# Optimization experiments

Hardware: AMD Instinct MI355X
Metric: run time of the kernel (lower is better)

## Reference

```python
import jax, jax.numpy as jnp
import numpy as np

N_EMBD = 768
N_HEAD = 12


def setup_inputs() -> dict:
    key = jax.random.key(0)
    ks = jax.random.split(key, 5)
    B, T, C = 2, 4096, N_EMBD
    s = 1.0 / np.sqrt(C)
    x = jax.random.normal(ks[0], (B, T, C), dtype=jnp.float32)
    w_attn = jax.random.normal(ks[1], (C, 3 * C), dtype=jnp.float32) * s
    b_attn = jnp.zeros((3 * C,), dtype=jnp.float32)
    w_proj = jax.random.normal(ks[2], (C, C), dtype=jnp.float32) * s
    b_proj = jnp.zeros((C,), dtype=jnp.float32)
    return {"x": x, "w_attn": w_attn, "b_attn": b_attn,
            "w_proj": w_proj, "b_proj": b_proj}


def reference(x, w_attn, b_attn, w_proj, b_proj):
    B, T, C = x.shape
    H = N_HEAD
    D = C // H  # head dim
    qkv = x @ w_attn + b_attn  # [B,T,3C]
    q, k, v = jnp.split(qkv, 3, axis=-1)
    # [B,H,T,D]
    q = q.reshape(B, T, H, D).transpose(0, 2, 1, 3)
    k = k.reshape(B, T, H, D).transpose(0, 2, 1, 3)
    v = v.reshape(B, T, H, D).transpose(0, 2, 1, 3)
    scale = 1.0 / jnp.sqrt(jnp.asarray(D, dtype=x.dtype))
    att = jnp.einsum('bhqd,bhkd->bhqk', q, k) * scale  # [B,H,T,T]
    causal = jnp.tril(jnp.ones((T, T), dtype=bool))
    att = jnp.where(causal[None, None], att, -jnp.inf)
    att = jax.nn.softmax(att, axis=-1)
    y = jnp.einsum('bhqk,bhkd->bhqd', att, v)  # [B,H,T,D]
    y = y.transpose(0, 2, 1, 3).reshape(B, T, C)
    return y @ w_proj + b_proj
```

## Files before the change

kernel.cpp:

```cpp
#include <hip/hip_runtime.h>

#define TSEQ 4096
#define CEMB 768
#define NHEAD 12

using bf16x8 = __attribute__((ext_vector_type(8))) short;
using f32x4  = __attribute__((ext_vector_type(4))) float;

#if __has_builtin(__builtin_amdgcn_exp2f)
#define EXP2(x) __builtin_amdgcn_exp2f(x)
#else
#define EXP2(x) exp2f(x)
#endif

__device__ __forceinline__ unsigned int f2bf(float f) {
    unsigned int u = __float_as_uint(f);
    return (u + 0x7fffu + ((u >> 16) & 1u)) >> 16;
}
__device__ __forceinline__ unsigned int f2bf_fast(float f) {
    return (__float_as_uint(f) + 0x8000u) >> 16;
}
__device__ __forceinline__ unsigned int cvt_pk_bf16(float lo, float hi) {
    unsigned int r;
    asm("v_cvt_pk_bf16_f32 %0, %1, %2" : "=v"(r) : "v"(lo), "v"(hi));
    return r;
}
__device__ __forceinline__ void pswap(unsigned int& d, unsigned int& s) {
    asm("v_permlane32_swap_b32 %0, %1" : "+v"(d), "+v"(s));
    asm("v_permlane16_swap_b32 %0, %1" : "+v"(d), "+v"(s));
}
__device__ __forceinline__ void async_cp16(void* lds, const void* g) {
    __builtin_amdgcn_global_load_lds(
        (const __attribute__((address_space(1))) void*)g,
        (__attribute__((address_space(3))) void*)lds, 16, 0, 0);
}

__global__ __launch_bounds__(256) void cvt_bf16(
    const float* __restrict__ X, unsigned short* __restrict__ Xb, int n8)
{
    int i = blockIdx.x * 256 + threadIdx.x;
    if (i >= n8) return;
    float4 a = *reinterpret_cast<const float4*>(&X[(size_t)i * 8]);
    float4 b = *reinterpret_cast<const float4*>(&X[(size_t)i * 8 + 4]);
    uint4 o;
    o.x = f2bf(a.x) | (f2bf(a.y) << 16);
    o.y = f2bf(a.z) | (f2bf(a.w) << 16);
    o.z = f2bf(b.x) | (f2bf(b.y) << 16);
    o.w = f2bf(b.z) | (f2bf(b.w) << 16);
    *reinterpret_cast<uint4*>(&Xb[(size_t)i * 8]) = o;
}

__global__ __launch_bounds__(256) void wtrans(
    const float* __restrict__ W, unsigned short* __restrict__ WT, int K, int N)
{
    __shared__ unsigned short tile[64][72];
    const int k0 = blockIdx.y * 64, n0 = blockIdx.x * 64;
    const int tid = threadIdx.x;
#pragma unroll
    for (int it = 0; it < 4; ++it) {
        int f = tid + it * 256;
        int r = f >> 4, c4 = f & 15;
        float4 v = *reinterpret_cast<const float4*>(&W[(size_t)(k0 + r) * N + n0 + c4 * 4]);
        tile[r][c4 * 4 + 0] = (unsigned short)f2bf(v.x);
        tile[r][c4 * 4 + 1] = (unsigned short)f2bf(v.y);
        tile[r][c4 * 4 + 2] = (unsigned short)f2bf(v.z);
        tile[r][c4 * 4 + 3] = (unsigned short)f2bf(v.w);
    }
    __syncthreads();
#pragma unroll
    for (int it = 0; it < 2; ++it) {
        int f = tid + it * 256;
        int rn = f >> 3, c8 = f & 7;
        unsigned short tmp[8];
#pragma unroll
        for (int j = 0; j < 8; ++j) tmp[j] = tile[c8 * 8 + j][rn];
        *reinterpret_cast<uint4*>(&WT[(size_t)(n0 + rn) * K + k0 + c8 * 8]) =
            *reinterpret_cast<uint4*>(tmp);
    }
}

template<int BF16OUT, int QSCALE, int VTRANS>
__global__ __launch_bounds__(256) void gemm_mfma(
    const unsigned short* __restrict__ A,
    const unsigned short* __restrict__ BT,
    const float* __restrict__ bias,
    void* __restrict__ Cv,
    unsigned short* __restrict__ VtG,
    int M, int N, int K)
{
    __shared__ __align__(16) unsigned short As[128 * 64];
    __shared__ __align__(16) unsigned short Bs[128 * 64];

    const int nwg = gridDim.x * gridDim.y;
    const int id = blockIdx.y * gridDim.x + blockIdx.x;
    const int qx = nwg >> 3;
    const int swz = (id & 7) * qx + (id >> 3);
    const int nb = N >> 7;
    const int m0 = (swz / nb) * 128, n0 = (swz % nb) * 128;

    const int tid = threadIdx.x;
    const int w = tid >> 6, lane = tid & 63;
    const int wr = w >> 1, wc = w & 1;
    const int lq = lane & 15, g = lane >> 4;
    const int wrOff = wr * 64, wcOff = wc * 64;

    f32x4 acc[4][4];
#pragma unroll
    for (int i = 0; i < 4; ++i)
#pragma unroll
        for (int j = 0; j < 4; ++j) acc[i][j] = (f32x4){0.f, 0.f, 0.f, 0.f};

    for (int k0 = 0; k0 < K; k0 += 64) {
#pragma unroll
        for (int it = 0; it < 4; ++it) {
            const int dbase = it * 256 + w * 64;
            const int d = dbase + lane;
            const int r = d >> 3;
            const int s = (d & 7) ^ (r & 7);
            async_cp16((char*)As + dbase * 16, A + (size_t)(m0 + r) * K + k0 + s * 8);
            async_cp16((char*)Bs + dbase * 16, BT + (size_t)(n0 + r) * K + k0 + s * 8);
        }
        __syncthreads();

#pragma unroll
        for (int kk = 0; kk < 2; ++kk) {
            bf16x8 af[4], bfr[4];
#pragma unroll
            for (int i = 0; i < 4; ++i) {
                const int ra = wrOff + i * 16 + lq;
                af[i] = *reinterpret_cast<const bf16x8*>(
                    (char*)As + ra * 128 + (((kk * 4 + g) ^ (ra & 7)) << 4));
                const int rb = wcOff + i * 16 + lq;
                bfr[i] = *reinterpret_cast<const bf16x8*>(
                    (char*)Bs + rb * 128 + (((kk * 4 + g) ^ (rb & 7)) << 4));
            }
#pragma unroll
            for (int i = 0; i < 4; ++i)
#pragma unroll
                for (int j = 0; j < 4; ++j)
                    acc[i][j] = __builtin_amdgcn_mfma_f32_16x16x32_bf16(
                        af[i], bfr[j], acc[i][j], 0, 0, 0);
        }
        __syncthreads();
    }

#pragma unroll
    for (int i = 0; i < 4; ++i)
#pragma unroll
        for (int j = 0; j < 4; ++j) {
            const int col = n0 + wcOff + j * 16 + lq;
            const float bv = bias[col];
            const float scl = (QSCALE && col < CEMB) ? 0.18033688011112042f : 1.0f;
            const int row0 = m0 + wrOff + i * 16 + g * 4;
            float v0 = (acc[i][j][0] + bv) * scl;
            float v1 = (acc[i][j][1] + bv) * scl;
            float v2 = (acc[i][j][2] + bv) * scl;
            float v3 = (acc[i][j][3] + bv) * scl;
            if (VTRANS && col >= 2 * CEMB) {
                const int hh = (col - 2 * CEMB) >> 6;
                const int dd = col & 63;
                uint2 pk;
                pk.x = f2bf(v0) | (f2bf(v1) << 16);
                pk.y = f2bf(v2) | (f2bf(v3) << 16);
                *reinterpret_cast<uint2*>(
                    &VtG[((size_t)(row0 >> 12) * NHEAD + hh) * 64 * TSEQ +
                         (size_t)dd * TSEQ + (row0 & 4095)]) = pk;
            } else if (BF16OUT) {
                unsigned short* Cb = (unsigned short*)Cv;
                Cb[(size_t)(row0 + 0) * N + col] = (unsigned short)f2bf(v0);
                Cb[(size_t)(row0 + 1) * N + col] = (unsigned short)f2bf(v1);
                Cb[(size_t)(row0 + 2) * N + col] = (unsigned short)f2bf(v2);
                Cb[(size_t)(row0 + 3) * N + col] = (unsigned short)f2bf(v3);
            } else {
                float* Cf = (float*)Cv;
                Cf[(size_t)(row0 + 0) * N + col] = v0;
                Cf[(size_t)(row0 + 1) * N + col] = v1;
                Cf[(size_t)(row0 + 2) * N + col] = v2;
                Cf[(size_t)(row0 + 3) * N + col] = v3;
            }
        }
}


#define QK_DUAL(SA, SB)                                                               \
{                                                                                     \
    const int xr = lq & 7;                                                            \
    _Pragma("unroll")                                                                 \
    for (int c = 0; c < 4; ++c) {                                                     \
        const int krow = 16 * c + lq;                                                 \
        bf16x8 kf0 = *reinterpret_cast<const bf16x8*>(Kb + krow * 128 + ((g ^ xr) << 4));       \
        bf16x8 kf1 = *reinterpret_cast<const bf16x8*>(Kb + krow * 128 + (((4 + g) ^ xr) << 4)); \
        f32x4 a = (f32x4){0.f, 0.f, 0.f, 0.f};                                        \
        a = __builtin_amdgcn_mfma_f32_16x16x32_bf16(kf0, qfA[0], a, 0, 0, 0);         \
        a = __builtin_amdgcn_mfma_f32_16x16x32_bf16(kf1, qfA[1], a, 0, 0, 0);         \
        SA[c] = a;                                                                    \
        f32x4 bb = (f32x4){0.f, 0.f, 0.f, 0.f};                                       \
        bb = __builtin_amdgcn_mfma_f32_16x16x32_bf16(kf0, qfB[0], bb, 0, 0, 0);       \
        bb = __builtin_amdgcn_mfma_f32_16x16x32_bf16(kf1, qfB[1], bb, 0, 0, 0);       \
        SB[c] = bb;                                                                   \
    }                                                                                 \
}

#define QK_ONE(SB, QF)                                                                \
{                                                                                     \
    const int xr = lq & 7;                                                            \
    _Pragma("unroll")                                                                 \
    for (int c = 0; c < 4; ++c) {                                                     \
        const int krow = 16 * c + lq;                                                 \
        bf16x8 kf0 = *reinterpret_cast<const bf16x8*>(Kb + krow * 128 + ((g ^ xr) << 4));       \
        bf16x8 kf1 = *reinterpret_cast<const bf16x8*>(Kb + krow * 128 + (((4 + g) ^ xr) << 4)); \
        f32x4 a = (f32x4){0.f, 0.f, 0.f, 0.f};                                        \
        a = __builtin_amdgcn_mfma_f32_16x16x32_bf16(kf0, QF[0], a, 0, 0, 0);          \
        a = __builtin_amdgcn_mfma_f32_16x16x32_bf16(kf1, QF[1], a, 0, 0, 0);          \
        SB[c] = a;                                                                    \
    }                                                                                 \
}

#define MASK_TILE(SFR)                                                                \
{                                                                                     \
    const int qloc = 16 * w + lq;                                                     \
    _Pragma("unroll")                                                                 \
    for (int c = 0; c < 4; ++c)                                                       \
        _Pragma("unroll")                                                             \
        for (int r = 0; r < 4; ++r)                                                   \
            if (16 * c + 4 * g + r > qloc) SFR[c][r] = -1e30f;                        \
}

#define SM_TILE(SFR, MM, LL, OO)                                                      \
{                                                                                     \
    float mx = SFR[0][0];                                                             \
    _Pragma("unroll")                                                                 \
    for (int c = 0; c < 4; ++c)                                                       \
        _Pragma("unroll")                                                             \
        for (int r = 0; r < 4; ++r) mx = fmaxf(mx, SFR[c][r]);                        \
    mx = fmaxf(mx, __shfl_xor(mx, 16));                                               \
    mx = fmaxf(mx, __shfl_xor(mx, 32));                                               \
    const float mnew = fmaxf(MM, mx);                                                 \
    const float al = EXP2(MM - mnew);                                                 \
    MM = mnew;                                                                        \
    float rs = 0.f;                                                                   \
    _Pragma("unroll")                                                                 \
    for (int c = 0; c < 4; ++c)                                                       \
        _Pragma("unroll")                                                             \
        for (int r = 0; r < 4; ++r) {                                                 \
            const float p = EXP2(SFR[c][r] - MM);                                     \
            SFR[c][r] = p;                                                            \
            rs += p;                                                                  \
        }                                                                             \
    rs += __shfl_xor(rs, 16);                                                         \
    rs += __shfl_xor(rs, 32);                                                         \
    LL = al * LL + rs;                                                                \
    _Pragma("unroll")                                                                 \
    for (int dt = 0; dt < 4; ++dt) OO[dt] *= al;                                      \
}

#define P_EXCH(SFR, PF0, PF1)                                                         \
{                                                                                     \
    unsigned int w00 = cvt_pk_bf16(SFR[0][0], SFR[0][1]);                             \
    unsigned int w01 = cvt_pk_bf16(SFR[0][2], SFR[0][3]);                             \
    unsigned int w10 = cvt_pk_bf16(SFR[1][0], SFR[1][1]);                             \
    unsigned int w11 = cvt_pk_bf16(SFR[1][2], SFR[1][3]);                             \
    unsigned int w20 = cvt_pk_bf16(SFR[2][0], SFR[2][1]);                             \
    unsigned int w21 = cvt_pk_bf16(SFR[2][2], SFR[2][3]);                             \
    unsigned int w30 = cvt_pk_bf16(SFR[3][0], SFR[3][1]);                             \
    unsigned int w31 = cvt_pk_bf16(SFR[3][2], SFR[3][3]);                             \
    uint4 p0, p1;                                                                     \
    { unsigned int d = w00, s = w10; pswap(d, s); p0.x = d; p0.z = s; }               \
    { unsigned int d = w01, s = w11; pswap(d, s); p0.y = d; p0.w = s; }               \
    { unsigned int d = w20, s = w30; pswap(d, s); p1.x = d; p1.z = s; }               \
    { unsigned int d = w21, s = w31; pswap(d, s); p1.y = d; p1.w = s; }               \
    PF0 = __builtin_bit_cast(bf16x8, p0);                                             \
    PF1 = __builtin_bit_cast(bf16x8, p1);                                             \
}

#define PV_DUAL(OA, OB, PA0, PA1, PB0, PB1)                                           \
{                                                                                     \
    const int xq = lq & 7;                                                            \
    _Pragma("unroll")                                                                 \
    for (int dt = 0; dt < 4; ++dt) {                                                  \
        const int vrow = 16 * dt + lq;                                                \
        bf16x8 vf0 = *reinterpret_cast<const bf16x8*>(Vb + vrow * 128 + ((g ^ xq) << 4));       \
        bf16x8 vf1 = *reinterpret_cast<const bf16x8*>(Vb + vrow * 128 + (((4 + g) ^ xq) << 4)); \
        OA[dt] = __builtin_amdgcn_mfma_f32_16x16x32_bf16(vf0, PA0, OA[dt], 0, 0, 0);  \
        OA[dt] = __builtin_amdgcn_mfma_f32_16x16x32_bf16(vf1, PA1, OA[dt], 0, 0, 0);  \
        OB[dt] = __builtin_amdgcn_mfma_f32_16x16x32_bf16(vf0, PB0, OB[dt], 0, 0, 0);  \
        OB[dt] = __builtin_amdgcn_mfma_f32_16x16x32_bf16(vf1, PB1, OB[dt], 0, 0, 0);  \
    }                                                                                 \
}

#define PV_ONE(OB, PB0, PB1)                                                          \
{                                                                                     \
    const int xq = lq & 7;                                                            \
    _Pragma("unroll")                                                                 \
    for (int dt = 0; dt < 4; ++dt) {                                                  \
        const int vrow = 16 * dt + lq;                                                \
        bf16x8 vf0 = *reinterpret_cast<const bf16x8*>(Vb + vrow * 128 + ((g ^ xq) << 4));       \
        bf16x8 vf1 = *reinterpret_cast<const bf16x8*>(Vb + vrow * 128 + (((4 + g) ^ xq) << 4)); \
        OB[dt] = __builtin_amdgcn_mfma_f32_16x16x32_bf16(vf0, PB0, OB[dt], 0, 0, 0);  \
        OB[dt] = __builtin_amdgcn_mfma_f32_16x16x32_bf16(vf1, PB1, OB[dt], 0, 0, 0);  \
    }                                                                                 \
}

#define STAGE_KV(KT, BUF)                                                             \
{                                                                                     \
    const int kn = (KT) * 64;                                                         \
    _Pragma("unroll")                                                                 \
    for (int it = 0; it < 2; ++it) {                                                  \
        const int dbase = it * 256 + w * 64;                                          \
        const int d = dbase + lane;                                                   \
        const int r = d >> 3;                                                         \
        const int s = (d & 7) ^ (r & 7);                                              \
        async_cp16(Kl[BUF] + dbase * 16, qkvB + (rowBase + kn + r) * 2304 + kOff + s * 8); \
        async_cp16(Vl[BUF] + dbase * 16, Vhead + (size_t)r * TSEQ + kn + s * 8);      \
    }                                                                                 \
}

__global__ __launch_bounds__(256, 3) void attn_mfma12(
    const unsigned short* __restrict__ qkvB,
    const unsigned short* __restrict__ VtG,
    unsigned short* __restrict__ Yb)
{
    __shared__ __align__(16) char Kl[2][8192];
    __shared__ __align__(16) char Vl[2][8192];

    const int NT = TSEQ / 64;
    const int id = blockIdx.x;
    const int xcd = id & 7;
    const int local = id >> 3;
    const int bh = xcd * 3 + (local % 3);
    const int qtA = local / 3;
    const int qtB = NT - 1 - qtA;

    const int b = bh / NHEAD, h = bh % NHEAD;
    const int tid = threadIdx.x;
    const int w = tid >> 6, lane = tid & 63;
    const int g = lane >> 4, lq = lane & 15;

    const size_t rowBase = (size_t)b * TSEQ;
    const int kOff = CEMB + h * 64;
    const unsigned short* Vhead = VtG + (size_t)bh * 64 * TSEQ;

    bf16x8 qfA[2], qfB[2];
    {
        const size_t rA = rowBase + (size_t)qtA * 64 + 16 * w + lq;
        const size_t rB = rowBase + (size_t)qtB * 64 + 16 * w + lq;
#pragma unroll
        for (int dt = 0; dt < 2; ++dt) {
            qfA[dt] = *reinterpret_cast<const bf16x8*>(&qkvB[rA * 2304 + h * 64 + 32 * dt + 8 * g]);
            qfB[dt] = *reinterpret_cast<const bf16x8*>(&qkvB[rB * 2304 + h * 64 + 32 * dt + 8 * g]);
        }
    }

    f32x4 oA[4], oB[4];
    float mA = -1e30f, lA = 0.f, mB = -1e30f, lB = 0.f;
#pragma unroll
    for (int dt = 0; dt < 4; ++dt) {
        oA[dt] = (f32x4){0.f, 0.f, 0.f, 0.f};
        oB[dt] = (f32x4){0.f, 0.f, 0.f, 0.f};
    }

    STAGE_KV(0, 0);

    for (int kt = 0; kt <= qtA; ++kt) {
        const int cur = kt & 1;
        __syncthreads();
        STAGE_KV(kt + 1, cur ^ 1);
        const char* Kb = Kl[cur];
        const char* Vb = Vl[cur];

        f32x4 sA[4], sB[4];
        QK_DUAL(sA, sB);
        if (kt == qtA) MASK_TILE(sA);
        SM_TILE(sA, mA, lA, oA);
        SM_TILE(sB, mB, lB, oB);
        bf16x8 pA0, pA1, pB0, pB1;
        P_EXCH(sA, pA0, pA1);
        P_EXCH(sB, pB0, pB1);
        PV_DUAL(oA, oB, pA0, pA1, pB0, pB1);
    }

    for (int kt = qtA + 1; kt <= qtB; ++kt) {
        const int cur = kt & 1;
        __syncthreads();
        if (kt < qtB) STAGE_KV(kt + 1, cur ^ 1);
        const char* Kb = Kl[cur];
        const char* Vb = Vl[cur];

        f32x4 sB[4];
        QK_ONE(sB, qfB);
        if (kt == qtB) MASK_TILE(sB);
        SM_TILE(sB, mB, lB, oB);
        bf16x8 pB0, pB1;
        P_EXCH(sB, pB0, pB1);
        PV_ONE(oB, pB0, pB1);
    }

    const float invA = 1.f / lA;
    const float invB = 1.f / lB;
    const size_t rowA = rowBase + (size_t)qtA * 64 + 16 * w + lq;
    const size_t rowB = rowBase + (size_t)qtB * 64 + 16 * w + lq;
#pragma unroll
    for (int dt = 0; dt < 4; ++dt) {
        uint2 a, bb;
        a.x  = f2bf_fast(oA[dt][0] * invA) | (f2bf_fast(oA[dt][1] * invA) << 16);
        a.y  = f2bf_fast(oA[dt][2] * invA) | (f2bf_fast(oA[dt][3] * invA) << 16);
        bb.x = f2bf_fast(oB[dt][0] * invB) | (f2bf_fast(oB[dt][1] * invB) << 16);
        bb.y = f2bf_fast(oB[dt][2] * invB) | (f2bf_fast(oB[dt][3] * invB) << 16);
        *reinterpret_cast<uint2*>(&Yb[rowA * CEMB + h * 64 + 16 * dt + 4 * g]) = a;
        *reinterpret_cast<uint2*>(&Yb[rowB * CEMB + h * 64 + 16 * dt + 4 * g]) = bb;
    }
}

extern "C" void kernel_launch(void* const* d_in, const int* in_sizes, int n_in,
                              void* d_out, int out_size, void* d_ws, size_t ws_size,
                              hipStream_t stream)
{
    const float* x      = (const float*)d_in[0];
    const float* w_attn = (const float*)d_in[1];
    const float* b_attn = (const float*)d_in[2];
    const float* w_proj = (const float*)d_in[3];
    const float* b_proj = (const float*)d_in[4];
    float* out = (float*)d_out;

    const int M = 2 * TSEQ;
    char* ws = (char*)d_ws;
    unsigned short* qkvB = (unsigned short*)ws;
    unsigned short* VtG  = (unsigned short*)(ws + 37748736);
    unsigned short* xYb  = (unsigned short*)(ws + 50331648);
    unsigned short* wT   = (unsigned short*)(ws + 62914560);
    unsigned short* wpT  = (unsigned short*)(ws + 66453504);

    cvt_bf16<<<dim3((M * CEMB) / 8 / 256), 256, 0, stream>>>(x, xYb, (M * CEMB) / 8);
    wtrans<<<dim3(3 * CEMB / 64, CEMB / 64), 256, 0, stream>>>(w_attn, wT, CEMB, 3 * CEMB);
    wtrans<<<dim3(CEMB / 64, CEMB / 64), 256, 0, stream>>>(w_proj, wpT, CEMB, CEMB);

    gemm_mfma<1, 1, 1><<<dim3(3 * CEMB / 128, M / 128), 256, 0, stream>>>(
        xYb, wT, b_attn, qkvB, VtG, M, 3 * CEMB, CEMB);

    attn_mfma12<<<dim3(768), 256, 0, stream>>>(qkvB, VtG, xYb);

    gemm_mfma<0, 0, 0><<<dim3(CEMB / 128, M / 128), 256, 0, stream>>>(
        xYb, wpT, b_proj, out, nullptr, M, CEMB, CEMB);
}
```

Baseline: 170.5 us.

## Replace paired causal q-tile blocks with one q-tile per block, heaviest first

The attention kernel previously gave each block two query tiles (qtA and its mirror 63-qtA) to balance causal work, sharing each K/V tile load between them. Now each block handles a single query tile, the grid doubles to 1536 blocks ordered from the longest tile down, and launch bounds rise from 3 to 5 blocks per CU. The aim is better occupancy and fewer live registers, relying on descending-work scheduling to balance load. In exchange, each K/V tile is now staged into shared memory once per query tile instead of once per pair, which roughly doubles LDS traffic for K/V, and the tail may be less balanced.

```diff
diff --git a/kernel.cpp b/kernel.cpp
--- a/kernel.cpp
+++ b/kernel.cpp
@@ -182,25 +182,6 @@
 }
 
 
-#define QK_DUAL(SA, SB)                                                               \
-{                                                                                     \
-    const int xr = lq & 7;                                                            \
-    _Pragma("unroll")                                                                 \
-    for (int c = 0; c < 4; ++c) {                                                     \
-        const int krow = 16 * c + lq;                                                 \
-        bf16x8 kf0 = *reinterpret_cast<const bf16x8*>(Kb + krow * 128 + ((g ^ xr) << 4));       \
-        bf16x8 kf1 = *reinterpret_cast<const bf16x8*>(Kb + krow * 128 + (((4 + g) ^ xr) << 4)); \
-        f32x4 a = (f32x4){0.f, 0.f, 0.f, 0.f};                                        \
-        a = __builtin_amdgcn_mfma_f32_16x16x32_bf16(kf0, qfA[0], a, 0, 0, 0);         \
-        a = __builtin_amdgcn_mfma_f32_16x16x32_bf16(kf1, qfA[1], a, 0, 0, 0);         \
-        SA[c] = a;                                                                    \
-        f32x4 bb = (f32x4){0.f, 0.f, 0.f, 0.f};                                       \
-        bb = __builtin_amdgcn_mfma_f32_16x16x32_bf16(kf0, qfB[0], bb, 0, 0, 0);       \
-        bb = __builtin_amdgcn_mfma_f32_16x16x32_bf16(kf1, qfB[1], bb, 0, 0, 0);       \
-        SB[c] = bb;                                                                   \
-    }                                                                                 \
-}
-
 #define QK_ONE(SB, QF)                                                                \
 {                                                                                     \
     const int xr = lq & 7;                                                            \
@@ -264,28 +245,13 @@
     unsigned int w21 = cvt_pk_bf16(SFR[2][2], SFR[2][3]);                             \
     unsigned int w30 = cvt_pk_bf16(SFR[3][0], SFR[3][1]);                             \
     unsigned int w31 = cvt_pk_bf16(SFR[3][2], SFR[3][3]);                             \
-    uint4 p0, p1;                                                                     \
-    { unsigned int d = w00, s = w10; pswap(d, s); p0.x = d; p0.z = s; }               \
-    { unsigned int d = w01, s = w11; pswap(d, s); p0.y = d; p0.w = s; }               \
-    { unsigned int d = w20, s = w30; pswap(d, s); p1.x = d; p1.z = s; }               \
-    { unsigned int d = w21, s = w31; pswap(d, s); p1.y = d; p1.w = s; }               \
-    PF0 = __builtin_bit_cast(bf16x8, p0);                                             \
-    PF1 = __builtin_bit_cast(bf16x8, p1);                                             \
-}
-
-#define PV_DUAL(OA, OB, PA0, PA1, PB0, PB1)                                           \
-{                                                                                     \
-    const int xq = lq & 7;                                                            \
-    _Pragma("unroll")                                                                 \
-    for (int dt = 0; dt < 4; ++dt) {                                                  \
-        const int vrow = 16 * dt + lq;                                                \
-        bf16x8 vf0 = *reinterpret_cast<const bf16x8*>(Vb + vrow * 128 + ((g ^ xq) << 4));       \
-        bf16x8 vf1 = *reinterpret_cast<const bf16x8*>(Vb + vrow * 128 + (((4 + g) ^ xq) << 4)); \
-        OA[dt] = __builtin_amdgcn_mfma_f32_16x16x32_bf16(vf0, PA0, OA[dt], 0, 0, 0);  \
-        OA[dt] = __builtin_amdgcn_mfma_f32_16x16x32_bf16(vf1, PA1, OA[dt], 0, 0, 0);  \
-        OB[dt] = __builtin_amdgcn_mfma_f32_16x16x32_bf16(vf0, PB0, OB[dt], 0, 0, 0);  \
-        OB[dt] = __builtin_amdgcn_mfma_f32_16x16x32_bf16(vf1, PB1, OB[dt], 0, 0, 0);  \
-    }                                                                                 \
+    uint4 q0_, q1_;                                                                   \
+    { unsigned int d = w00, s = w10; pswap(d, s); q0_.x = d; q0_.z = s; }             \
+    { unsigned int d = w01, s = w11; pswap(d, s); q0_.y = d; q0_.w = s; }             \
+    { unsigned int d = w20, s = w30; pswap(d, s); q1_.x = d; q1_.z = s; }             \
+    { unsigned int d = w21, s = w31; pswap(d, s); q1_.y = d; q1_.w = s; }             \
+    PF0 = __builtin_bit_cast(bf16x8, q0_);                                            \
+    PF1 = __builtin_bit_cast(bf16x8, q1_);                                            \
 }
 
 #define PV_ONE(OB, PB0, PB1)                                                          \
@@ -315,7 +281,7 @@
     }                                                                                 \
 }
 
-__global__ __launch_bounds__(256, 3) void attn_mfma12(
+__global__ __launch_bounds__(256, 5) void attn_mfma13(
     const unsigned short* __restrict__ qkvB,
     const unsigned short* __restrict__ VtG,
     unsigned short* __restrict__ Yb)
@@ -323,13 +289,11 @@
     __shared__ __align__(16) char Kl[2][8192];
     __shared__ __align__(16) char Vl[2][8192];
 
-    const int NT = TSEQ / 64;
     const int id = blockIdx.x;
     const int xcd = id & 7;
     const int local = id >> 3;
     const int bh = xcd * 3 + (local % 3);
-    const int qtA = local / 3;
-    const int qtB = NT - 1 - qtA;
+    const int qt = 63 - local / 3;
 
     const int b = bh / NHEAD, h = bh % NHEAD;
     const int tid = threadIdx.x;
@@ -340,74 +304,45 @@
     const int kOff = CEMB + h * 64;
     const unsigned short* Vhead = VtG + (size_t)bh * 64 * TSEQ;
 
-    bf16x8 qfA[2], qfB[2];
+    bf16x8 qf[2];
     {
-        const size_t rA = rowBase + (size_t)qtA * 64 + 16 * w + lq;
-        const size_t rB = rowBase + (size_t)qtB * 64 + 16 * w + lq;
-#pragma unroll
-        for (int dt = 0; dt < 2; ++dt) {
-            qfA[dt] = *reinterpret_cast<const bf16x8*>(&qkvB[rA * 2304 + h * 64 + 32 * dt + 8 * g]);
-            qfB[dt] = *reinterpret_cast<const bf16x8*>(&qkvB[rB * 2304 + h * 64 + 32 * dt + 8 * g]);
-        }
-    }
-
-    f32x4 oA[4], oB[4];
-    float mA = -1e30f, lA = 0.f, mB = -1e30f, lB = 0.f;
-#pragma unroll
-    for (int dt = 0; dt < 4; ++dt) {
-        oA[dt] = (f32x4){0.f, 0.f, 0.f, 0.f};
-        oB[dt] = (f32x4){0.f, 0.f, 0.f, 0.f};
-    }
+        const size_t rQ = rowBase + (size_t)qt * 64 + 16 * w + lq;
+#pragma unroll
+        for (int dt = 0; dt < 2; ++dt)
+            qf[dt] = *reinterpret_cast<const bf16x8*>(&qkvB[rQ * 2304 + h * 64 + 32 * dt + 8 * g]);
+    }
+
+    f32x4 o[4];
+    float m = -1e30f, l = 0.f;
+#pragma unroll
+    for (int dt = 0; dt < 4; ++dt) o[dt] = (f32x4){0.f, 0.f, 0.f, 0.f};
 
     STAGE_KV(0, 0);
 
-    for (int kt = 0; kt <= qtA; ++kt) {
+    for (int kt = 0; kt <= qt; ++kt) {
         const int cur = kt & 1;
         __syncthreads();
-        STAGE_KV(kt + 1, cur ^ 1);
+        if (kt < qt) STAGE_KV(kt + 1, cur ^ 1);
         const char* Kb = Kl[cur];
         const char* Vb = Vl[cur];
 
-        f32x4 sA[4], sB[4];
-        QK_DUAL(sA, sB);
-        if (kt == qtA) MASK_TILE(sA);
-        SM_TILE(sA, mA, lA, oA);
-        SM_TILE(sB, mB, lB, oB);
-        bf16x8 pA0, pA1, pB0, pB1;
-        P_EXCH(sA, pA0, pA1);
-        P_EXCH(sB, pB0, pB1);
-        PV_DUAL(oA, oB, pA0, pA1, pB0, pB1);
-    }
-
-    for (int kt = qtA + 1; kt <= qtB; ++kt) {
-        const int cur = kt & 1;
-        __syncthreads();
-        if (kt < qtB) STAGE_KV(kt + 1, cur ^ 1);
-        const char* Kb = Kl[cur];
-        const char* Vb = Vl[cur];
-
-        f32x4 sB[4];
-        QK_ONE(sB, qfB);
-        if (kt == qtB) MASK_TILE(sB);
-        SM_TILE(sB, mB, lB, oB);
-        bf16x8 pB0, pB1;
-        P_EXCH(sB, pB0, pB1);
-        PV_ONE(oB, pB0, pB1);
-    }
-
-    const float invA = 1.f / lA;
-    const float invB = 1.f / lB;
-    const size_t rowA = rowBase + (size_t)qtA * 64 + 16 * w + lq;
-    const size_t rowB = rowBase + (size_t)qtB * 64 + 16 * w + lq;
+        f32x4 s[4];
+        QK_ONE(s, qf);
+        if (kt == qt) MASK_TILE(s);
+        SM_TILE(s, m, l, o);
+        bf16x8 pe0, pe1;
+        P_EXCH(s, pe0, pe1);
+        PV_ONE(o, pe0, pe1);
+    }
+
+    const float inv = 1.f / l;
+    const size_t row = rowBase + (size_t)qt * 64 + 16 * w + lq;
 #pragma unroll
     for (int dt = 0; dt < 4; ++dt) {
-        uint2 a, bb;
-        a.x  = f2bf_fast(oA[dt][0] * invA) | (f2bf_fast(oA[dt][1] * invA) << 16);
-        a.y  = f2bf_fast(oA[dt][2] * invA) | (f2bf_fast(oA[dt][3] * invA) << 16);
-        bb.x = f2bf_fast(oB[dt][0] * invB) | (f2bf_fast(oB[dt][1] * invB) << 16);
-        bb.y = f2bf_fast(oB[dt][2] * invB) | (f2bf_fast(oB[dt][3] * invB) << 16);
-        *reinterpret_cast<uint2*>(&Yb[rowA * CEMB + h * 64 + 16 * dt + 4 * g]) = a;
-        *reinterpret_cast<uint2*>(&Yb[rowB * CEMB + h * 64 + 16 * dt + 4 * g]) = bb;
+        uint2 a;
+        a.x = f2bf_fast(o[dt][0] * inv) | (f2bf_fast(o[dt][1] * inv) << 16);
+        a.y = f2bf_fast(o[dt][2] * inv) | (f2bf_fast(o[dt][3] * inv) << 16);
+        *reinterpret_cast<uint2*>(&Yb[row * CEMB + h * 64 + 16 * dt + 4 * g]) = a;
     }
 }
 
@@ -437,7 +372,7 @@
     gemm_mfma<1, 1, 1><<<dim3(3 * CEMB / 128, M / 128), 256, 0, stream>>>(
         xYb, wT, b_attn, qkvB, VtG, M, 3 * CEMB, CEMB);
 
-    attn_mfma12<<<dim3(768), 256, 0, stream>>>(qkvB, VtG, xYb);
+    attn_mfma13<<<dim3(1536), 256, 0, stream>>>(qkvB, VtG, xYb);
 
     gemm_mfma<0, 0, 0><<<dim3(CEMB / 128, M / 128), 256, 0, stream>>>(
         xYb, wpT, b_proj, out, nullptr, M, CEMB, CEMB);
```

After: 175.3 us. +2.8%, slower.
